# Kernel tuning notes

Hardware: AMD Instinct MI355X
Metric: run time of the kernel (lower is better)

The kernel has to match this reference:

```python
import jax, jax.numpy as jnp
import numpy as np
import math

B, S, E, H = 2, 2048, 2048, 16
HD = E // H // 2  # 64, per-head dim of each differential half
DEPTH = 12
LAMBDA_INIT = 0.8 - 0.6 * math.exp(-0.3 * DEPTH)
EPS = 1e-5


def setup_inputs() -> dict:
    key = jax.random.key(0)
    ks = jax.random.split(key, 10)
    sc = 0.02
    return {
        "x": jax.random.normal(ks[0], (B, S, E), jnp.float32),
        "Wq": jax.random.normal(ks[1], (E, E), jnp.float32) * sc,
        "Wk": jax.random.normal(ks[2], (E, E), jnp.float32) * sc,
        "Wv": jax.random.normal(ks[3], (E, E), jnp.float32) * sc,
        "Wo": jax.random.normal(ks[4], (E, E), jnp.float32) * sc,
        "lambda_q1": jax.random.normal(ks[5], (HD,), jnp.float32) * 0.1,
        "lambda_k1": jax.random.normal(ks[6], (HD,), jnp.float32) * 0.1,
        "lambda_q2": jax.random.normal(ks[7], (HD,), jnp.float32) * 0.1,
        "lambda_k2": jax.random.normal(ks[8], (HD,), jnp.float32) * 0.1,
        "gamma": jnp.ones((2 * HD,), jnp.float32),
    }


def _rope_interleaved(x, cos, sin):
    # x: [b, s, h, d]; cos/sin: [s, d//2]; pairs are (0,1),(2,3),...
    xe, xo = x[..., 0::2], x[..., 1::2]
    c = cos[None, :, None, :]
    s = sin[None, :, None, :]
    oe = xe * c - xo * s
    oo = xe * s + xo * c
    return jnp.stack([oe, oo], axis=-1).reshape(x.shape)


def reference(x, Wq, Wk, Wv, Wo, lambda_q1, lambda_k1, lambda_q2, lambda_k2, gamma):
    b, t, _ = x.shape
    # rotary tables (rotary dim == HD, interleaved)
    angle = 1.0 / 10000 ** jnp.linspace(0.0, 1.0, HD // 2, dtype=jnp.float32)
    freqs = jnp.arange(t, dtype=jnp.float32)[:, None] * angle  # [t, HD//2]
    cos, sin = jnp.cos(freqs), jnp.sin(freqs)

    q = (x @ Wq.T).reshape(b, t, 2 * H, HD)
    k = (x @ Wk.T).reshape(b, t, 2 * H, HD)
    v = (x @ Wv.T).reshape(b, t, H, 2 * HD)  # concat(v1, v2) along last dim

    q = _rope_interleaved(q, cos, sin)
    k = _rope_interleaved(k, cos, sin)

    q = q.reshape(b, t, H, 2, HD)
    k = k.reshape(b, t, H, 2, HD)
    q1, q2 = q[:, :, :, 0], q[:, :, :, 1]
    k1, k2 = k[:, :, :, 0], k[:, :, :, 1]

    scale = HD ** -0.5  # flash_attn default softmax scale
    # branch 1: softmax(q1 k1) @ [v1|v2]
    s1 = jnp.einsum("bthd,bshd->bhts", q1, k1) * scale
    p1 = jax.nn.softmax(s1, axis=-1)
    o1 = jnp.einsum("bhts,bshd->bthd", p1, v)  # [b,t,H,2*HD]
    # branch 2: softmax(q2 k2) @ [v1|v2]
    s2 = jnp.einsum("bthd,bshd->bhts", q2, k2) * scale
    p2 = jax.nn.softmax(s2, axis=-1)
    o2 = jnp.einsum("bhts,bshd->bthd", p2, v)

    lam1 = jnp.exp(jnp.sum(lambda_q1 * lambda_k1))
    lam2 = jnp.exp(jnp.sum(lambda_q2 * lambda_k2))
    lam = lam1 - lam2 + LAMBDA_INIT

    attn = o1 - lam * o2  # [b,t,H,2*HD]
    # RMSNorm over last dim (2*HD) with affine gamma
    rms = jax.lax.rsqrt(jnp.mean(attn * attn, axis=-1, keepdims=True) + EPS)
    attn = attn * rms * gamma
    attn = attn * (1.0 - LAMBDA_INIT)
    attn = attn.reshape(b, t, H * 2 * HD)
    return attn @ Wo.T
```

## Files before the change

kernel.cpp:

```cpp
#include <hip/hip_runtime.h>
#include <cstdint>
#include <cstddef>

typedef unsigned short u16;
typedef __attribute__((ext_vector_type(8))) short short8;
typedef __attribute__((ext_vector_type(4))) float f32x4;
typedef __attribute__((ext_vector_type(16))) float f32x16;

#define MFMA_B16(a,b,c) __builtin_amdgcn_mfma_f32_16x16x32_bf16((a),(b),(c),0,0,0)
#define MFMA32(a,b,c)  __builtin_amdgcn_mfma_f32_32x32x16_bf16((a),(b),(c),0,0,0)

#define S_LEN 2048
#define EMB 2048
#define QKV_N 6144
#define HD 64
#define LAMBDA_INIT_F 0.78360576653162f
#define ONE_MINUS_LI 0.21639423346838f
#define EXP2_SCALE 0.18033688011112042f

static __device__ __forceinline__ u16 f2bf(float f) {
  unsigned u = __float_as_uint(f);
  unsigned r = ((u >> 16) & 1u) + 0x7fffu;
  return (u16)((u + r) >> 16);
}
static __device__ __forceinline__ float bf2f(u16 h) {
  return __uint_as_float(((unsigned)h) << 16);
}
static __device__ __forceinline__ unsigned cvt_pk_bf16(float lo, float hi) {
  unsigned r;
  asm("v_cvt_pk_bf16_f32 %0, %1, %2" : "=v"(r) : "v"(lo), "v"(hi));
  return r;
}
static __device__ __forceinline__ void gload_lds16(const u16* g, u16* l) {
  __builtin_amdgcn_global_load_lds((const __attribute__((address_space(1))) void*)g,
                                   (__attribute__((address_space(3))) void*)l, 16, 0, 0);
}

__global__ void cvt_f32_bf16(const float* __restrict__ s, u16* __restrict__ d, int n4) {
  int i = blockIdx.x * 256 + threadIdx.x;
  if (i >= n4) return;
  f32x4 v = *(const f32x4*)&s[i * 4];
  unsigned lo = cvt_pk_bf16(v[0], v[1]);
  unsigned hi = cvt_pk_bf16(v[2], v[3]);
  *(unsigned long long*)&d[i * 4] = (unsigned long long)lo | ((unsigned long long)hi << 32);
}

template <int BF16OUT>
__global__ __launch_bounds__(256, 2) void gemm_bt(const u16* __restrict__ A,
                                                  const u16* __restrict__ B,
                                                  void* __restrict__ Cout,
                                                  int M, int N, int K) {
  __shared__ u16 As[128 * 32];
  __shared__ u16 Bs[128 * 32];
  const int tid = threadIdx.x;
  const int lane = tid & 63, wv = tid >> 6;
  const int bm = blockIdx.x * 128, bn = blockIdx.y * 128;
  const int wr = (wv >> 1) * 64, wc = (wv & 1) * 64;
  const int lr = lane & 15, hk = lane >> 4;

  const int r0 = tid >> 2;
  const int c0 = (tid & 3) * 8;
  const u16* ga = A + (size_t)(bm + r0) * K + c0;
  const u16* gb = B + (size_t)(bn + r0) * K + c0;
  const size_t rstep = (size_t)64 * K;

  f32x4 acc[4][4] = {};

  for (int k0 = 0; k0 < K; k0 += 32) {
    __syncthreads();
    gload_lds16(ga + k0,         &As[(tid) * 8]);
    gload_lds16(ga + rstep + k0, &As[(tid + 256) * 8]);
    gload_lds16(gb + k0,         &Bs[(tid) * 8]);
    gload_lds16(gb + rstep + k0, &Bs[(tid + 256) * 8]);
    __syncthreads();
    short8 af[4], bfv[4];
#pragma unroll
    for (int i = 0; i < 4; i++) af[i] = *(const short8*)&As[(wr + i * 16 + lr) * 32 + hk * 8];
#pragma unroll
    for (int j = 0; j < 4; j++) bfv[j] = *(const short8*)&Bs[(wc + j * 16 + lr) * 32 + hk * 8];
#pragma unroll
    for (int i = 0; i < 4; i++)
#pragma unroll
      for (int j = 0; j < 4; j++)
        acc[i][j] = MFMA_B16(af[i], bfv[j], acc[i][j]);
  }

  if (BF16OUT) {
    u16* C = (u16*)Cout;
#pragma unroll
    for (int i = 0; i < 4; i++)
#pragma unroll
      for (int j = 0; j < 4; j++)
#pragma unroll
        for (int r = 0; r < 4; r++) {
          int row = bm + wr + i * 16 + hk * 4 + r;
          int col = bn + wc + j * 16 + lr;
          C[(size_t)row * N + col] = f2bf(acc[i][j][r]);
        }
  } else {
    float* C = (float*)Cout;
#pragma unroll
    for (int i = 0; i < 4; i++)
#pragma unroll
      for (int j = 0; j < 4; j++)
#pragma unroll
        for (int r = 0; r < 4; r++) {
          int row = bm + wr + i * 16 + hk * 4 + r;
          int col = bn + wc + j * 16 + lr;
          C[(size_t)row * N + col] = acc[i][j][r];
        }
  }
}

__global__ void rope_kernel(u16* __restrict__ qkv) {
  int idx = blockIdx.x * 256 + threadIdx.x;
  int p = idx & 31;
  int u = (idx >> 5) & 63;
  int m = idx >> 11;
  int t = m & (S_LEN - 1);
  int col = (u < 32) ? (u * 64 + 2 * p) : (EMB + (u - 32) * 64 + 2 * p);
  u16* ptr = qkv + (size_t)m * QKV_N + col;
  unsigned v = *(unsigned*)ptr;
  float xe = bf2f((u16)(v & 0xffff));
  float xo = bf2f((u16)(v >> 16));
  float w = expf((float)p * (-9.210340371976184f / 31.0f));
  float ang = (float)t * w;
  float sn, cs;
  sincosf(ang, &sn, &cs);
  float oe = xe * cs - xo * sn;
  float oo = xe * sn + xo * cs;
  *(unsigned*)ptr = (unsigned)f2bf(oe) | (((unsigned)f2bf(oo)) << 16);
}

#define SW(row, colByte) ((((row)) << 7) + ((colByte) ^ (((row) & 7) << 4)))

#define QKT(Kc, Q0, Q1, Q2, Q3, KT, Pc, LSUM)                                    \
  do {                                                                           \
    f32x16 s = {};                                                               \
    s = MFMA32(*(const short8*)((Kc) + SW((KT) * 32 + l31, 0  + hi16)), Q0, s);  \
    s = MFMA32(*(const short8*)((Kc) + SW((KT) * 32 + l31, 32 + hi16)), Q1, s);  \
    s = MFMA32(*(const short8*)((Kc) + SW((KT) * 32 + l31, 64 + hi16)), Q2, s);  \
    s = MFMA32(*(const short8*)((Kc) + SW((KT) * 32 + l31, 96 + hi16)), Q3, s);  \
    _Pragma("unroll") for (int r = 0; r < 16; r += 4) {                          \
      float e0 = __builtin_amdgcn_exp2f(s[r]     * EXP2_SCALE);                  \
      float e1 = __builtin_amdgcn_exp2f(s[r + 1] * EXP2_SCALE);                  \
      float e2 = __builtin_amdgcn_exp2f(s[r + 2] * EXP2_SCALE);                  \
      float e3 = __builtin_amdgcn_exp2f(s[r + 3] * EXP2_SCALE);                  \
      LSUM += (e0 + e1) + (e2 + e3);                                             \
      unsigned lo_ = cvt_pk_bf16(e0, e1);                                        \
      unsigned hi_ = cvt_pk_bf16(e2, e3);                                        \
      *(unsigned long long*)((Pc) + SW(l31, (KT) * 64 + (r >> 2) * 16 + hi8)) =  \
          (unsigned long long)lo_ | ((unsigned long long)hi_ << 32);             \
    }                                                                            \
  } while (0)

#define PVD(DT, O1, O2)                                                          \
  do {                                                                           \
    short8 va0 = *(const short8*)(VTc + SW((DT) * 32 + l31, 0  + hi16));         \
    short8 va1 = *(const short8*)(VTc + SW((DT) * 32 + l31, 32 + hi16));         \
    short8 va2 = *(const short8*)(VTc + SW((DT) * 32 + l31, 64 + hi16));         \
    short8 va3 = *(const short8*)(VTc + SW((DT) * 32 + l31, 96 + hi16));         \
    O1 = MFMA32(va0, p1f0, O1); O1 = MFMA32(va1, p1f1, O1);                      \
    O1 = MFMA32(va2, p1f2, O1); O1 = MFMA32(va3, p1f3, O1);                      \
    O2 = MFMA32(va0, p2f0, O2); O2 = MFMA32(va1, p2f1, O2);                      \
    O2 = MFMA32(va2, p2f2, O2); O2 = MFMA32(va3, p2f3, O2);                      \
  } while (0)

__global__ __launch_bounds__(256, 2) void attn_kernel(
    const u16* __restrict__ qkv, u16* __restrict__ attnb,
    const float* __restrict__ lq1, const float* __restrict__ lk1,
    const float* __restrict__ lq2, const float* __restrict__ lk2,
    const float* __restrict__ gamma) {
  __shared__ u16 K1s[64 * 64];
  __shared__ u16 K2s[64 * 64];
  __shared__ u16 VTs[128 * 64];
  __shared__ u16 Ps[2 * 2 * 32 * 64];
  __shared__ float Lr[2][2][2][32];
  __shared__ float Sr[2][2][32];

  const int g = blockIdx.x;
  const int xcd = g & 7;
  const int gi = g >> 3;
  const int bh = xcd * 4 + (gi >> 5);
  const int qt = gi & 31;
  const int b = bh >> 4, h = bh & 15;

  const int tid = threadIdx.x, lane = tid & 63, wv = tid >> 6;
  const int qg = wv >> 1;
  const int dh = wv & 1;
  const int l31 = lane & 31;
  const int hi16 = (lane >> 5) * 16;
  const int hi8 = (lane >> 5) * 8;
  const int hi4 = (lane >> 5) * 4;

  float d1 = lq1[lane] * lk1[lane];
  float d2 = lq2[lane] * lk2[lane];
#pragma unroll
  for (int off = 32; off; off >>= 1) { d1 += __shfl_xor(d1, off); d2 += __shfl_xor(d2, off); }
  const float lam = __expf(d1) - __expf(d2) + LAMBDA_INIT_F;

  const int qbase = qt * 64 + qg * 32;
  const u16* qp1 = qkv + (size_t)(b * S_LEN + qbase + l31) * QKV_N + (2 * h) * 64;
  const u16* qp2 = qp1 + 64;
  short8 q1f0 = *(const short8*)(qp1 + hi8);
  short8 q1f1 = *(const short8*)(qp1 + 16 + hi8);
  short8 q1f2 = *(const short8*)(qp1 + 32 + hi8);
  short8 q1f3 = *(const short8*)(qp1 + 48 + hi8);
  short8 q2f0 = *(const short8*)(qp2 + hi8);
  short8 q2f1 = *(const short8*)(qp2 + 16 + hi8);
  short8 q2f2 = *(const short8*)(qp2 + 32 + hi8);
  short8 q2f3 = *(const short8*)(qp2 + 48 + hi8);

  f32x16 o1t0 = {}, o1t1 = {}, o2t0 = {}, o2t1 = {};
  float l1p = 0.f, l2p = 0.f;

  const int gl_row = wv * 8 + (lane >> 3);
  const int gl_cb  = ((lane & 7) ^ (lane >> 3)) * 8;
  u16* k1d = &K1s[(wv * 8) * 64 + lane * 8];
  u16* k2d = &K2s[(wv * 8) * 64 + lane * 8];

  const int vkv = (tid & 31) * 2;
  const int vd0 = (tid >> 5) * 8;

  const u16* kb1 = qkv + (size_t)b * S_LEN * QKV_N + EMB + (2 * h) * 64;
  const u16* kb2 = kb1 + 64;
  const u16* vbp = qkv + (size_t)b * S_LEN * QKV_N + 2 * EMB + h * 128;

  char* K1c = (char*)K1s;
  char* K2c = (char*)K2s;
  char* VTc = (char*)VTs;
  char* P1c = (char*)&Ps[(qg * 2 + 0) * 32 * 64];
  char* P2c = (char*)&Ps[(qg * 2 + 1) * 32 * 64];

  for (int kv0 = 0; kv0 < S_LEN; kv0 += 64) {
    __syncthreads();
    {
      const u16* g1 = kb1 + (size_t)(kv0 + gl_row) * QKV_N + gl_cb;
      const u16* g2 = kb2 + (size_t)(kv0 + gl_row) * QKV_N + gl_cb;
      gload_lds16(g1, k1d);
      gload_lds16(g1 + (size_t)32 * QKV_N, k1d + 32 * 64);
      gload_lds16(g2, k2d);
      gload_lds16(g2 + (size_t)32 * QKV_N, k2d + 32 * 64);
    }
    {
      const u16* vs = vbp + (size_t)(kv0 + vkv) * QKV_N + vd0;
      short8 a0 = *(const short8*)vs;
      short8 a1 = *(const short8*)(vs + QKV_N);
      short8 b0 = *(const short8*)(vs + 64);
      short8 b1 = *(const short8*)(vs + QKV_N + 64);
#pragma unroll
      for (int j = 0; j < 8; j++) {
        unsigned pk0 = (unsigned)(u16)a0[j] | (((unsigned)(u16)a1[j]) << 16);
        *(unsigned*)(VTc + SW(vd0 + j, vkv * 2)) = pk0;
        unsigned pk1 = (unsigned)(u16)b0[j] | (((unsigned)(u16)b1[j]) << 16);
        *(unsigned*)(VTc + SW(vd0 + 64 + j, vkv * 2)) = pk1;
      }
    }
    __syncthreads();

    QKT(K1c, q1f0, q1f1, q1f2, q1f3, dh, P1c, l1p);
    QKT(K2c, q2f0, q2f1, q2f2, q2f3, dh, P2c, l2p);
    __syncthreads();

    short8 p1f0 = *(const short8*)(P1c + SW(l31, 0  + hi16));
    short8 p1f1 = *(const short8*)(P1c + SW(l31, 32 + hi16));
    short8 p1f2 = *(const short8*)(P1c + SW(l31, 64 + hi16));
    short8 p1f3 = *(const short8*)(P1c + SW(l31, 96 + hi16));
    short8 p2f0 = *(const short8*)(P2c + SW(l31, 0  + hi16));
    short8 p2f1 = *(const short8*)(P2c + SW(l31, 32 + hi16));
    short8 p2f2 = *(const short8*)(P2c + SW(l31, 64 + hi16));
    short8 p2f3 = *(const short8*)(P2c + SW(l31, 96 + hi16));

    PVD(dh * 2 + 0, o1t0, o2t0);
    PVD(dh * 2 + 1, o1t1, o2t1);
  }

  float l1 = l1p + __shfl_xor(l1p, 32);
  float l2 = l2p + __shfl_xor(l2p, 32);
  if (lane < 32) { Lr[qg][0][dh][l31] = l1; Lr[qg][1][dh][l31] = l2; }
  __syncthreads();
  const float inv1 = 1.f / (Lr[qg][0][0][l31] + Lr[qg][0][1][l31]);
  const float inv2 = 1.f / (Lr[qg][1][0][l31] + Lr[qg][1][1][l31]);

  float ss = 0.f;
#define COMB(O1, O2)                                                   \
  _Pragma("unroll") for (int i = 0; i < 16; i++) {                     \
    float a = O1[i] * inv1 - lam * (O2[i] * inv2);                     \
    O1[i] = a;                                                         \
    ss += a * a;                                                       \
  }
  COMB(o1t0, o2t0) COMB(o1t1, o2t1)
#undef COMB
  ss += __shfl_xor(ss, 32);
  if (lane < 32) Sr[qg][dh][l31] = ss;
  __syncthreads();
  const float SS = Sr[qg][0][l31] + Sr[qg][1][l31];
  const float sc2 = rsqrtf(SS * (1.f / 128.f) + 1e-5f) * ONE_MINUS_LI;

  u16* orow = attnb + (size_t)(b * S_LEN + qbase + l31) * EMB + h * 128;
#define WRT(O1, DT)                                                             \
  _Pragma("unroll") for (int gg = 0; gg < 4; gg++) {                            \
    int d = dh * 64 + (DT) * 32 + gg * 8 + hi4;                                 \
    f32x4 gv = *(const f32x4*)&gamma[d];                                        \
    unsigned wlo = cvt_pk_bf16(O1[4 * gg] * gv[0] * sc2, O1[4 * gg + 1] * gv[1] * sc2); \
    unsigned whi = cvt_pk_bf16(O1[4 * gg + 2] * gv[2] * sc2, O1[4 * gg + 3] * gv[3] * sc2); \
    *(unsigned long long*)&orow[d] = (unsigned long long)wlo | ((unsigned long long)whi << 32); \
  }
  WRT(o1t0, 0) WRT(o1t1, 1)
#undef WRT
}

extern "C" void kernel_launch(void* const* d_in, const int* in_sizes, int n_in,
                              void* d_out, int out_size, void* d_ws, size_t ws_size,
                              hipStream_t stream) {
  (void)in_sizes; (void)n_in; (void)out_size; (void)ws_size;
  const float* x   = (const float*)d_in[0];
  const float* Wq  = (const float*)d_in[1];
  const float* Wk  = (const float*)d_in[2];
  const float* Wv  = (const float*)d_in[3];
  const float* Wo  = (const float*)d_in[4];
  const float* lq1 = (const float*)d_in[5];
  const float* lk1 = (const float*)d_in[6];
  const float* lq2 = (const float*)d_in[7];
  const float* lk2 = (const float*)d_in[8];
  const float* gam = (const float*)d_in[9];

  char* ws = (char*)d_ws;
  u16* xb    = (u16*)(ws);
  u16* Wcat  = (u16*)(ws + 16777216);
  u16* Wob   = (u16*)(ws + 41943040);
  u16* qkv   = (u16*)(ws + 50331648);
  u16* attnb = xb;

  const int NE = EMB * EMB;
  cvt_f32_bf16<<<(2 * NE / 4 + 255) / 256, 256, 0, stream>>>(x, xb, 2 * NE / 4);
  cvt_f32_bf16<<<(NE / 4 + 255) / 256, 256, 0, stream>>>(Wq, Wcat, NE / 4);
  cvt_f32_bf16<<<(NE / 4 + 255) / 256, 256, 0, stream>>>(Wk, Wcat + NE, NE / 4);
  cvt_f32_bf16<<<(NE / 4 + 255) / 256, 256, 0, stream>>>(Wv, Wcat + 2 * NE, NE / 4);
  cvt_f32_bf16<<<(NE / 4 + 255) / 256, 256, 0, stream>>>(Wo, Wob, NE / 4);

  dim3 g1(4096 / 128, QKV_N / 128);
  gemm_bt<1><<<g1, 256, 0, stream>>>(xb, Wcat, qkv, 4096, QKV_N, EMB);

  rope_kernel<<<(4096 * 64 * 32) / 256, 256, 0, stream>>>(qkv);

  attn_kernel<<<1024, 256, 0, stream>>>(qkv, attnb, lq1, lk1, lq2, lk2, gam);

  dim3 g2(4096 / 128, EMB / 128);
  gemm_bt<0><<<g2, 256, 0, stream>>>(attnb, Wob, d_out, 4096, EMB, EMB);
}
```

Measured before the change: 355.5 us.

## Load K fragments directly from global, prefetch V, set MFMA priority

K tiles are now read straight from global memory into registers per wave instead of being staged through LDS with async loads, which removes the K shared buffers and one barrier per iteration. V loads for the next tile are issued at the end of the current iteration (register prefetch) to overlap global latency with compute. s_setprio is raised around MFMA sequences. The trade-off is that each K row is fetched redundantly by multiple waves (both query groups), relying on L1/L2 hits, and register pressure rises.

```diff
diff --git a/kernel.cpp b/kernel.cpp
--- a/kernel.cpp
+++ b/kernel.cpp
@@ -134,13 +134,20 @@
 
 #define SW(row, colByte) ((((row)) << 7) + ((colByte) ^ (((row) & 7) << 4)))
 
-#define QKT(Kc, Q0, Q1, Q2, Q3, KT, Pc, LSUM)                                    \
+#define QKT_G(kbp, Q0, Q1, Q2, Q3, Pc, LSUM)                                     \
   do {                                                                           \
+    const u16* kr_ = (kbp) + (size_t)(kv0 + dh * 32 + l31) * QKV_N + hi8;        \
+    short8 k0_ = *(const short8*)(kr_);                                          \
+    short8 k1_ = *(const short8*)(kr_ + 16);                                     \
+    short8 k2_ = *(const short8*)(kr_ + 32);                                     \
+    short8 k3_ = *(const short8*)(kr_ + 48);                                     \
     f32x16 s = {};                                                               \
-    s = MFMA32(*(const short8*)((Kc) + SW((KT) * 32 + l31, 0  + hi16)), Q0, s);  \
-    s = MFMA32(*(const short8*)((Kc) + SW((KT) * 32 + l31, 32 + hi16)), Q1, s);  \
-    s = MFMA32(*(const short8*)((Kc) + SW((KT) * 32 + l31, 64 + hi16)), Q2, s);  \
-    s = MFMA32(*(const short8*)((Kc) + SW((KT) * 32 + l31, 96 + hi16)), Q3, s);  \
+    __builtin_amdgcn_s_setprio(1);                                               \
+    s = MFMA32(k0_, Q0, s);                                                      \
+    s = MFMA32(k1_, Q1, s);                                                      \
+    s = MFMA32(k2_, Q2, s);                                                      \
+    s = MFMA32(k3_, Q3, s);                                                      \
+    __builtin_amdgcn_s_setprio(0);                                               \
     _Pragma("unroll") for (int r = 0; r < 16; r += 4) {                          \
       float e0 = __builtin_amdgcn_exp2f(s[r]     * EXP2_SCALE);                  \
       float e1 = __builtin_amdgcn_exp2f(s[r + 1] * EXP2_SCALE);                  \
@@ -149,7 +156,7 @@
       LSUM += (e0 + e1) + (e2 + e3);                                             \
       unsigned lo_ = cvt_pk_bf16(e0, e1);                                        \
       unsigned hi_ = cvt_pk_bf16(e2, e3);                                        \
-      *(unsigned long long*)((Pc) + SW(l31, (KT) * 64 + (r >> 2) * 16 + hi8)) =  \
+      *(unsigned long long*)((Pc) + SW(l31, dh * 64 + (r >> 2) * 16 + hi8)) =    \
           (unsigned long long)lo_ | ((unsigned long long)hi_ << 32);             \
     }                                                                            \
   } while (0)
@@ -160,10 +167,12 @@
     short8 va1 = *(const short8*)(VTc + SW((DT) * 32 + l31, 32 + hi16));         \
     short8 va2 = *(const short8*)(VTc + SW((DT) * 32 + l31, 64 + hi16));         \
     short8 va3 = *(const short8*)(VTc + SW((DT) * 32 + l31, 96 + hi16));         \
+    __builtin_amdgcn_s_setprio(1);                                               \
     O1 = MFMA32(va0, p1f0, O1); O1 = MFMA32(va1, p1f1, O1);                      \
     O1 = MFMA32(va2, p1f2, O1); O1 = MFMA32(va3, p1f3, O1);                      \
     O2 = MFMA32(va0, p2f0, O2); O2 = MFMA32(va1, p2f1, O2);                      \
     O2 = MFMA32(va2, p2f2, O2); O2 = MFMA32(va3, p2f3, O2);                      \
+    __builtin_amdgcn_s_setprio(0);                                               \
   } while (0)
 
 __global__ __launch_bounds__(256, 2) void attn_kernel(
@@ -171,8 +180,6 @@
     const float* __restrict__ lq1, const float* __restrict__ lk1,
     const float* __restrict__ lq2, const float* __restrict__ lk2,
     const float* __restrict__ gamma) {
-  __shared__ u16 K1s[64 * 64];
-  __shared__ u16 K2s[64 * 64];
   __shared__ u16 VTs[128 * 64];
   __shared__ u16 Ps[2 * 2 * 32 * 64];
   __shared__ float Lr[2][2][2][32];
@@ -214,11 +221,6 @@
   f32x16 o1t0 = {}, o1t1 = {}, o2t0 = {}, o2t1 = {};
   float l1p = 0.f, l2p = 0.f;
 
-  const int gl_row = wv * 8 + (lane >> 3);
-  const int gl_cb  = ((lane & 7) ^ (lane >> 3)) * 8;
-  u16* k1d = &K1s[(wv * 8) * 64 + lane * 8];
-  u16* k2d = &K2s[(wv * 8) * 64 + lane * 8];
-
   const int vkv = (tid & 31) * 2;
   const int vd0 = (tid >> 5) * 8;
 
@@ -226,40 +228,33 @@
   const u16* kb2 = kb1 + 64;
   const u16* vbp = qkv + (size_t)b * S_LEN * QKV_N + 2 * EMB + h * 128;
 
-  char* K1c = (char*)K1s;
-  char* K2c = (char*)K2s;
   char* VTc = (char*)VTs;
   char* P1c = (char*)&Ps[(qg * 2 + 0) * 32 * 64];
   char* P2c = (char*)&Ps[(qg * 2 + 1) * 32 * 64];
 
+  short8 va0p, va1p, vb0p, vb1p;
+#define VLOAD(kv0_)                                                      \
+  do {                                                                   \
+    const u16* vs_ = vbp + (size_t)((kv0_) + vkv) * QKV_N + vd0;         \
+    va0p = *(const short8*)vs_;                                          \
+    va1p = *(const short8*)(vs_ + QKV_N);                                \
+    vb0p = *(const short8*)(vs_ + 64);                                   \
+    vb1p = *(const short8*)(vs_ + QKV_N + 64);                           \
+  } while (0)
+
+  VLOAD(0);
+
   for (int kv0 = 0; kv0 < S_LEN; kv0 += 64) {
     __syncthreads();
-    {
-      const u16* g1 = kb1 + (size_t)(kv0 + gl_row) * QKV_N + gl_cb;
-      const u16* g2 = kb2 + (size_t)(kv0 + gl_row) * QKV_N + gl_cb;
-      gload_lds16(g1, k1d);
-      gload_lds16(g1 + (size_t)32 * QKV_N, k1d + 32 * 64);
-      gload_lds16(g2, k2d);
-      gload_lds16(g2 + (size_t)32 * QKV_N, k2d + 32 * 64);
+#pragma unroll
+    for (int j = 0; j < 8; j++) {
+      unsigned pk0 = (unsigned)(u16)va0p[j] | (((unsigned)(u16)va1p[j]) << 16);
+      *(unsigned*)(VTc + SW(vd0 + j, vkv * 2)) = pk0;
+      unsigned pk1 = (unsigned)(u16)vb0p[j] | (((unsigned)(u16)vb1p[j]) << 16);
+      *(unsigned*)(VTc + SW(vd0 + 64 + j, vkv * 2)) = pk1;
     }
-    {
-      const u16* vs = vbp + (size_t)(kv0 + vkv) * QKV_N + vd0;
-      short8 a0 = *(const short8*)vs;
-      short8 a1 = *(const short8*)(vs + QKV_N);
-      short8 b0 = *(const short8*)(vs + 64);
-      short8 b1 = *(const short8*)(vs + QKV_N + 64);
-#pragma unroll
-      for (int j = 0; j < 8; j++) {
-        unsigned pk0 = (unsigned)(u16)a0[j] | (((unsigned)(u16)a1[j]) << 16);
-        *(unsigned*)(VTc + SW(vd0 + j, vkv * 2)) = pk0;
-        unsigned pk1 = (unsigned)(u16)b0[j] | (((unsigned)(u16)b1[j]) << 16);
-        *(unsigned*)(VTc + SW(vd0 + 64 + j, vkv * 2)) = pk1;
-      }
-    }
-    __syncthreads();
-
-    QKT(K1c, q1f0, q1f1, q1f2, q1f3, dh, P1c, l1p);
-    QKT(K2c, q2f0, q2f1, q2f2, q2f3, dh, P2c, l2p);
+    QKT_G(kb1, q1f0, q1f1, q1f2, q1f3, P1c, l1p);
+    QKT_G(kb2, q2f0, q2f1, q2f2, q2f3, P2c, l2p);
     __syncthreads();
 
     short8 p1f0 = *(const short8*)(P1c + SW(l31, 0  + hi16));
@@ -273,7 +268,10 @@
 
     PVD(dh * 2 + 0, o1t0, o2t0);
     PVD(dh * 2 + 1, o1t1, o2t1);
-  }
+
+    if (kv0 + 64 < S_LEN) VLOAD(kv0 + 64);
+  }
+#undef VLOAD
 
   float l1 = l1p + __shfl_xor(l1p, 32);
   float l2 = l2p + __shfl_xor(l2p, 32);
```

New measurement: 415.7 us. +16.9%, slower.

## Split attention waves by differential branch, keep K in registers, combine via LDS

Applied to the files above, without the earlier changes.

Work in the attention kernel is now split so each wave handles one differential branch (q1/k1 or q2/k2) across all 128 V columns, rather than both branches across half the V columns. K tiles are loaded straight from global memory into registers and prefetched one iteration ahead, which drops the K staging in LDS and one barrier per tile. The LDS swizzle changes to 8-byte granularity with split 64-bit loads. At the end, the branch-2 wave writes its normalized output to LDS and the branch-1 wave combines, applies RMSNorm and writes. This should cut LDS traffic and barriers, at the cost of more accumulator registers and a serialized epilogue.

```diff
diff --git a/kernel.cpp b/kernel.cpp
--- a/kernel.cpp
+++ b/kernel.cpp
@@ -30,6 +30,12 @@
   unsigned r;
   asm("v_cvt_pk_bf16_f32 %0, %1, %2" : "=v"(r) : "v"(lo), "v"(hi));
   return r;
+}
+static __device__ __forceinline__ short8 ld64p(const char* base, int o0, int o1) {
+  union { unsigned long long q[2]; short8 s; } x;
+  x.q[0] = *(const unsigned long long*)(base + o0);
+  x.q[1] = *(const unsigned long long*)(base + o1);
+  return x.s;
 }
 static __device__ __forceinline__ void gload_lds16(const u16* g, u16* l) {
   __builtin_amdgcn_global_load_lds((const __attribute__((address_space(1))) void*)g,
@@ -132,51 +138,15 @@
   *(unsigned*)ptr = (unsigned)f2bf(oe) | (((unsigned)f2bf(oo)) << 16);
 }
 
-#define SW(row, colByte) ((((row)) << 7) + ((colByte) ^ (((row) & 7) << 4)))
-
-#define QKT(Kc, Q0, Q1, Q2, Q3, KT, Pc, LSUM)                                    \
-  do {                                                                           \
-    f32x16 s = {};                                                               \
-    s = MFMA32(*(const short8*)((Kc) + SW((KT) * 32 + l31, 0  + hi16)), Q0, s);  \
-    s = MFMA32(*(const short8*)((Kc) + SW((KT) * 32 + l31, 32 + hi16)), Q1, s);  \
-    s = MFMA32(*(const short8*)((Kc) + SW((KT) * 32 + l31, 64 + hi16)), Q2, s);  \
-    s = MFMA32(*(const short8*)((Kc) + SW((KT) * 32 + l31, 96 + hi16)), Q3, s);  \
-    _Pragma("unroll") for (int r = 0; r < 16; r += 4) {                          \
-      float e0 = __builtin_amdgcn_exp2f(s[r]     * EXP2_SCALE);                  \
-      float e1 = __builtin_amdgcn_exp2f(s[r + 1] * EXP2_SCALE);                  \
-      float e2 = __builtin_amdgcn_exp2f(s[r + 2] * EXP2_SCALE);                  \
-      float e3 = __builtin_amdgcn_exp2f(s[r + 3] * EXP2_SCALE);                  \
-      LSUM += (e0 + e1) + (e2 + e3);                                             \
-      unsigned lo_ = cvt_pk_bf16(e0, e1);                                        \
-      unsigned hi_ = cvt_pk_bf16(e2, e3);                                        \
-      *(unsigned long long*)((Pc) + SW(l31, (KT) * 64 + (r >> 2) * 16 + hi8)) =  \
-          (unsigned long long)lo_ | ((unsigned long long)hi_ << 32);             \
-    }                                                                            \
-  } while (0)
-
-#define PVD(DT, O1, O2)                                                          \
-  do {                                                                           \
-    short8 va0 = *(const short8*)(VTc + SW((DT) * 32 + l31, 0  + hi16));         \
-    short8 va1 = *(const short8*)(VTc + SW((DT) * 32 + l31, 32 + hi16));         \
-    short8 va2 = *(const short8*)(VTc + SW((DT) * 32 + l31, 64 + hi16));         \
-    short8 va3 = *(const short8*)(VTc + SW((DT) * 32 + l31, 96 + hi16));         \
-    O1 = MFMA32(va0, p1f0, O1); O1 = MFMA32(va1, p1f1, O1);                      \
-    O1 = MFMA32(va2, p1f2, O1); O1 = MFMA32(va3, p1f3, O1);                      \
-    O2 = MFMA32(va0, p2f0, O2); O2 = MFMA32(va1, p2f1, O2);                      \
-    O2 = MFMA32(va2, p2f2, O2); O2 = MFMA32(va3, p2f3, O2);                      \
-  } while (0)
+#define SW8(row, colByte) ((((row)) << 7) + ((colByte) ^ (((row) & 15) << 3)))
 
 __global__ __launch_bounds__(256, 2) void attn_kernel(
     const u16* __restrict__ qkv, u16* __restrict__ attnb,
     const float* __restrict__ lq1, const float* __restrict__ lk1,
     const float* __restrict__ lq2, const float* __restrict__ lk2,
     const float* __restrict__ gamma) {
-  __shared__ u16 K1s[64 * 64];
-  __shared__ u16 K2s[64 * 64];
-  __shared__ u16 VTs[128 * 64];
-  __shared__ u16 Ps[2 * 2 * 32 * 64];
-  __shared__ float Lr[2][2][2][32];
-  __shared__ float Sr[2][2][32];
+  __shared__ f32x4 pool4[2048];
+  char* pool = (char*)pool4;
 
   const int g = blockIdx.x;
   const int xcd = g & 7;
@@ -187,7 +157,7 @@
 
   const int tid = threadIdx.x, lane = tid & 63, wv = tid >> 6;
   const int qg = wv >> 1;
-  const int dh = wv & 1;
+  const int sw = wv & 1;
   const int l31 = lane & 31;
   const int hi16 = (lane >> 5) * 16;
   const int hi8 = (lane >> 5) * 8;
@@ -200,48 +170,39 @@
   const float lam = __expf(d1) - __expf(d2) + LAMBDA_INIT_F;
 
   const int qbase = qt * 64 + qg * 32;
-  const u16* qp1 = qkv + (size_t)(b * S_LEN + qbase + l31) * QKV_N + (2 * h) * 64;
-  const u16* qp2 = qp1 + 64;
-  short8 q1f0 = *(const short8*)(qp1 + hi8);
-  short8 q1f1 = *(const short8*)(qp1 + 16 + hi8);
-  short8 q1f2 = *(const short8*)(qp1 + 32 + hi8);
-  short8 q1f3 = *(const short8*)(qp1 + 48 + hi8);
-  short8 q2f0 = *(const short8*)(qp2 + hi8);
-  short8 q2f1 = *(const short8*)(qp2 + 16 + hi8);
-  short8 q2f2 = *(const short8*)(qp2 + 32 + hi8);
-  short8 q2f3 = *(const short8*)(qp2 + 48 + hi8);
-
-  f32x16 o1t0 = {}, o1t1 = {}, o2t0 = {}, o2t1 = {};
-  float l1p = 0.f, l2p = 0.f;
-
-  const int gl_row = wv * 8 + (lane >> 3);
-  const int gl_cb  = ((lane & 7) ^ (lane >> 3)) * 8;
-  u16* k1d = &K1s[(wv * 8) * 64 + lane * 8];
-  u16* k2d = &K2s[(wv * 8) * 64 + lane * 8];
+  const u16* qp = qkv + (size_t)(b * S_LEN + qbase + l31) * QKV_N + (2 * h + sw) * 64;
+  short8 qf0 = *(const short8*)(qp + hi8);
+  short8 qf1 = *(const short8*)(qp + 16 + hi8);
+  short8 qf2 = *(const short8*)(qp + 32 + hi8);
+  short8 qf3 = *(const short8*)(qp + 48 + hi8);
+
+  f32x16 ot0 = {}, ot1 = {}, ot2 = {}, ot3 = {};
+  float lp = 0.f;
 
   const int vkv = (tid & 31) * 2;
   const int vd0 = (tid >> 5) * 8;
 
-  const u16* kb1 = qkv + (size_t)b * S_LEN * QKV_N + EMB + (2 * h) * 64;
-  const u16* kb2 = kb1 + 64;
+  const u16* kbs = qkv + (size_t)b * S_LEN * QKV_N + EMB + (2 * h + sw) * 64;
   const u16* vbp = qkv + (size_t)b * S_LEN * QKV_N + 2 * EMB + h * 128;
 
-  char* K1c = (char*)K1s;
-  char* K2c = (char*)K2s;
-  char* VTc = (char*)VTs;
-  char* P1c = (char*)&Ps[(qg * 2 + 0) * 32 * 64];
-  char* P2c = (char*)&Ps[(qg * 2 + 1) * 32 * 64];
+  char* VTc = pool;
+  char* Pc  = pool + 16384 + wv * 4096;
+
+  short8 ka00, ka01, ka02, ka03, ka10, ka11, ka12, ka13;
+#define KLOAD(kv0_)                                                          \
+  do {                                                                       \
+    const u16* kr0_ = kbs + (size_t)((kv0_) + l31) * QKV_N + hi8;            \
+    const u16* kr1_ = kbs + (size_t)((kv0_) + 32 + l31) * QKV_N + hi8;       \
+    ka00 = *(const short8*)(kr0_);      ka01 = *(const short8*)(kr0_ + 16);  \
+    ka02 = *(const short8*)(kr0_ + 32); ka03 = *(const short8*)(kr0_ + 48);  \
+    ka10 = *(const short8*)(kr1_);      ka11 = *(const short8*)(kr1_ + 16);  \
+    ka12 = *(const short8*)(kr1_ + 32); ka13 = *(const short8*)(kr1_ + 48);  \
+  } while (0)
+
+  KLOAD(0);
 
   for (int kv0 = 0; kv0 < S_LEN; kv0 += 64) {
     __syncthreads();
-    {
-      const u16* g1 = kb1 + (size_t)(kv0 + gl_row) * QKV_N + gl_cb;
-      const u16* g2 = kb2 + (size_t)(kv0 + gl_row) * QKV_N + gl_cb;
-      gload_lds16(g1, k1d);
-      gload_lds16(g1 + (size_t)32 * QKV_N, k1d + 32 * 64);
-      gload_lds16(g2, k2d);
-      gload_lds16(g2 + (size_t)32 * QKV_N, k2d + 32 * 64);
-    }
     {
       const u16* vs = vbp + (size_t)(kv0 + vkv) * QKV_N + vd0;
       short8 a0 = *(const short8*)vs;
@@ -251,63 +212,113 @@
 #pragma unroll
       for (int j = 0; j < 8; j++) {
         unsigned pk0 = (unsigned)(u16)a0[j] | (((unsigned)(u16)a1[j]) << 16);
-        *(unsigned*)(VTc + SW(vd0 + j, vkv * 2)) = pk0;
+        *(unsigned*)(VTc + SW8(vd0 + j, vkv * 2)) = pk0;
         unsigned pk1 = (unsigned)(u16)b0[j] | (((unsigned)(u16)b1[j]) << 16);
-        *(unsigned*)(VTc + SW(vd0 + 64 + j, vkv * 2)) = pk1;
+        *(unsigned*)(VTc + SW8(vd0 + 64 + j, vkv * 2)) = pk1;
       }
     }
+
+#define QKTK(K0, K1, K2, K3, KT)                                               \
+    do {                                                                       \
+      f32x16 s = {};                                                           \
+      s = MFMA32(K0, qf0, s);                                                  \
+      s = MFMA32(K1, qf1, s);                                                  \
+      s = MFMA32(K2, qf2, s);                                                  \
+      s = MFMA32(K3, qf3, s);                                                  \
+      _Pragma("unroll") for (int r = 0; r < 16; r += 4) {                      \
+        float e0 = __builtin_amdgcn_exp2f(s[r]     * EXP2_SCALE);              \
+        float e1 = __builtin_amdgcn_exp2f(s[r + 1] * EXP2_SCALE);              \
+        float e2 = __builtin_amdgcn_exp2f(s[r + 2] * EXP2_SCALE);              \
+        float e3 = __builtin_amdgcn_exp2f(s[r + 3] * EXP2_SCALE);              \
+        lp += (e0 + e1) + (e2 + e3);                                           \
+        unsigned lo_ = cvt_pk_bf16(e0, e1);                                    \
+        unsigned hi_ = cvt_pk_bf16(e2, e3);                                    \
+        *(unsigned long long*)(Pc + SW8(l31, (KT) * 64 + (r >> 2) * 16 + hi8)) = \
+            (unsigned long long)lo_ | ((unsigned long long)hi_ << 32);         \
+      }                                                                        \
+    } while (0)
+    QKTK(ka00, ka01, ka02, ka03, 0);
+    QKTK(ka10, ka11, ka12, ka13, 1);
+#undef QKTK
+
+    if (kv0 + 64 < S_LEN) KLOAD(kv0 + 64);
+
+    asm volatile("" ::: "memory");
+    short8 p0 = ld64p(Pc, SW8(l31, 0 + hi16),  SW8(l31, 8 + hi16));
+    short8 p1 = ld64p(Pc, SW8(l31, 32 + hi16), SW8(l31, 40 + hi16));
+    short8 p2 = ld64p(Pc, SW8(l31, 64 + hi16), SW8(l31, 72 + hi16));
+    short8 p3 = ld64p(Pc, SW8(l31, 96 + hi16), SW8(l31, 104 + hi16));
+
     __syncthreads();
 
-    QKT(K1c, q1f0, q1f1, q1f2, q1f3, dh, P1c, l1p);
-    QKT(K2c, q2f0, q2f1, q2f2, q2f3, dh, P2c, l2p);
-    __syncthreads();
-
-    short8 p1f0 = *(const short8*)(P1c + SW(l31, 0  + hi16));
-    short8 p1f1 = *(const short8*)(P1c + SW(l31, 32 + hi16));
-    short8 p1f2 = *(const short8*)(P1c + SW(l31, 64 + hi16));
-    short8 p1f3 = *(const short8*)(P1c + SW(l31, 96 + hi16));
-    short8 p2f0 = *(const short8*)(P2c + SW(l31, 0  + hi16));
-    short8 p2f1 = *(const short8*)(P2c + SW(l31, 32 + hi16));
-    short8 p2f2 = *(const short8*)(P2c + SW(l31, 64 + hi16));
-    short8 p2f3 = *(const short8*)(P2c + SW(l31, 96 + hi16));
-
-    PVD(dh * 2 + 0, o1t0, o2t0);
-    PVD(dh * 2 + 1, o1t1, o2t1);
-  }
-
-  float l1 = l1p + __shfl_xor(l1p, 32);
-  float l2 = l2p + __shfl_xor(l2p, 32);
-  if (lane < 32) { Lr[qg][0][dh][l31] = l1; Lr[qg][1][dh][l31] = l2; }
+#define PVD(DT, OT)                                                            \
+    do {                                                                       \
+      int rw = (DT) * 32 + l31;                                                \
+      short8 va0 = ld64p(VTc, SW8(rw, 0 + hi16),  SW8(rw, 8 + hi16));          \
+      short8 va1 = ld64p(VTc, SW8(rw, 32 + hi16), SW8(rw, 40 + hi16));         \
+      short8 va2 = ld64p(VTc, SW8(rw, 64 + hi16), SW8(rw, 72 + hi16));         \
+      short8 va3 = ld64p(VTc, SW8(rw, 96 + hi16), SW8(rw, 104 + hi16));        \
+      OT = MFMA32(va0, p0, OT);                                                \
+      OT = MFMA32(va1, p1, OT);                                                \
+      OT = MFMA32(va2, p2, OT);                                                \
+      OT = MFMA32(va3, p3, OT);                                                \
+    } while (0)
+    PVD(0, ot0);
+    PVD(1, ot1);
+    PVD(2, ot2);
+    PVD(3, ot3);
+#undef PVD
+  }
+#undef KLOAD
+
+  float l = lp + __shfl_xor(lp, 32);
+  const float inv = 1.f / l;
+
   __syncthreads();
-  const float inv1 = 1.f / (Lr[qg][0][0][l31] + Lr[qg][0][1][l31]);
-  const float inv2 = 1.f / (Lr[qg][1][0][l31] + Lr[qg][1][1][l31]);
-
-  float ss = 0.f;
-#define COMB(O1, O2)                                                   \
-  _Pragma("unroll") for (int i = 0; i < 16; i++) {                     \
-    float a = O1[i] * inv1 - lam * (O2[i] * inv2);                     \
-    O1[i] = a;                                                         \
-    ss += a * a;                                                       \
-  }
-  COMB(o1t0, o2t0) COMB(o1t1, o2t1)
-#undef COMB
-  ss += __shfl_xor(ss, 32);
-  if (lane < 32) Sr[qg][dh][l31] = ss;
+  char* O2b = pool + qg * 16384;
+  if (sw == 1) {
+#define O2WR(OT, DT)                                                           \
+    _Pragma("unroll") for (int gg = 0; gg < 4; gg++) {                         \
+      int dB = ((DT) * 32 + gg * 8 + hi4) * 4;                                 \
+      f32x4 v_;                                                                \
+      v_[0] = OT[4 * gg] * inv;     v_[1] = OT[4 * gg + 1] * inv;              \
+      v_[2] = OT[4 * gg + 2] * inv; v_[3] = OT[4 * gg + 3] * inv;              \
+      *(f32x4*)(O2b + l31 * 512 + (dB ^ (l31 << 4))) = v_;                     \
+    }
+    O2WR(ot0, 0) O2WR(ot1, 1) O2WR(ot2, 2) O2WR(ot3, 3)
+#undef O2WR
+  }
   __syncthreads();
-  const float SS = Sr[qg][0][l31] + Sr[qg][1][l31];
-  const float sc2 = rsqrtf(SS * (1.f / 128.f) + 1e-5f) * ONE_MINUS_LI;
-
-  u16* orow = attnb + (size_t)(b * S_LEN + qbase + l31) * EMB + h * 128;
-#define WRT(O1, DT)                                                             \
-  _Pragma("unroll") for (int gg = 0; gg < 4; gg++) {                            \
-    int d = dh * 64 + (DT) * 32 + gg * 8 + hi4;                                 \
-    f32x4 gv = *(const f32x4*)&gamma[d];                                        \
-    unsigned wlo = cvt_pk_bf16(O1[4 * gg] * gv[0] * sc2, O1[4 * gg + 1] * gv[1] * sc2); \
-    unsigned whi = cvt_pk_bf16(O1[4 * gg + 2] * gv[2] * sc2, O1[4 * gg + 3] * gv[3] * sc2); \
-    *(unsigned long long*)&orow[d] = (unsigned long long)wlo | ((unsigned long long)whi << 32); \
-  }
-  WRT(o1t0, 0) WRT(o1t1, 1)
+  if (sw == 0) {
+    float ss = 0.f;
+#define COMBR(OT, DT)                                                          \
+    _Pragma("unroll") for (int gg = 0; gg < 4; gg++) {                         \
+      int dB = ((DT) * 32 + gg * 8 + hi4) * 4;                                 \
+      f32x4 o2 = *(const f32x4*)(O2b + l31 * 512 + (dB ^ (l31 << 4)));         \
+      float a0 = OT[4 * gg]     * inv - lam * o2[0];                           \
+      float a1 = OT[4 * gg + 1] * inv - lam * o2[1];                           \
+      float a2 = OT[4 * gg + 2] * inv - lam * o2[2];                           \
+      float a3 = OT[4 * gg + 3] * inv - lam * o2[3];                           \
+      OT[4 * gg] = a0; OT[4 * gg + 1] = a1; OT[4 * gg + 2] = a2; OT[4 * gg + 3] = a3; \
+      ss += (a0 * a0 + a1 * a1) + (a2 * a2 + a3 * a3);                         \
+    }
+    COMBR(ot0, 0) COMBR(ot1, 1) COMBR(ot2, 2) COMBR(ot3, 3)
+#undef COMBR
+    ss += __shfl_xor(ss, 32);
+    const float sc2 = rsqrtf(ss * (1.f / 128.f) + 1e-5f) * ONE_MINUS_LI;
+
+    u16* orow = attnb + (size_t)(b * S_LEN + qbase + l31) * EMB + h * 128;
+#define WRT(OT, DT)                                                            \
+    _Pragma("unroll") for (int gg = 0; gg < 4; gg++) {                         \
+      int d = (DT) * 32 + gg * 8 + hi4;                                        \
+      f32x4 gv = *(const f32x4*)&gamma[d];                                     \
+      unsigned wlo = cvt_pk_bf16(OT[4 * gg] * gv[0] * sc2, OT[4 * gg + 1] * gv[1] * sc2); \
+      unsigned whi = cvt_pk_bf16(OT[4 * gg + 2] * gv[2] * sc2, OT[4 * gg + 3] * gv[3] * sc2); \
+      *(unsigned long long*)&orow[d] = (unsigned long long)wlo | ((unsigned long long)whi << 32); \
+    }
+    WRT(ot0, 0) WRT(ot1, 1) WRT(ot2, 2) WRT(ot3, 3)
 #undef WRT
+  }
 }
 
 extern "C" void kernel_launch(void* const* d_in, const int* in_sizes, int n_in,
```

Result: slower. 391.1 us (+10.0%).
